# Performance work log

Measured on AMD Instinct MI355X. Metric: run time of the kernel, lower is better.

Reference implementation:

```python
import jax, jax.numpy as jnp
import numpy as np

EPS = 1e-5  # torch LayerNorm default

def _ln(x):
    # LayerNorm over last dim, no affine (elementwise_affine=False)
    m = jnp.mean(x, axis=-1, keepdims=True)
    v = jnp.var(x, axis=-1, keepdims=True)
    return (x - m) / jnp.sqrt(v + EPS)

def _build_orthogonal(phi):
    """Orthogonal matrix of the 'X' RBS circuit on d qubits (unary subspace).
    phi has 2d-3 angles: a descending diagonal of d-1 adjacent Givens rotations
    followed by an ascending diagonal of d-2. Each RBS(theta) acts on coords
    (k, k+1) as [[cos, sin], [-sin, cos]]."""
    d = (phi.shape[0] + 3) // 2
    W = jnp.eye(d, dtype=phi.dtype)
    wires = list(range(d - 1)) + list(range(d - 3, -1, -1))  # 2d-3 gates
    for g, k in enumerate(wires):
        c, s = jnp.cos(phi[g]), jnp.sin(phi[g])
        rk, rk1 = W[k], W[k + 1]
        W = W.at[k].set(c * rk + s * rk1)
        W = W.at[k + 1].set(-s * rk + c * rk1)
    return W

def setup_inputs() -> dict:
    key = jax.random.key(0)
    ks = jax.random.split(key, 8)
    B, N, E, H, dh = 16, 1024, 512, 8, 64
    return {
        "x": jax.random.normal(ks[0], (B, N, E), jnp.float32),
        "Wv": jax.random.normal(ks[1], (H, dh, dh), jnp.float32) / np.sqrt(dh).astype(np.float32),
        "bv": jnp.zeros((H, dh), jnp.float32),
        "phi": jax.random.uniform(ks[2], (H, 2 * dh - 3), jnp.float32, 0.0, 2.0 * np.pi),
        "W1": jax.random.normal(ks[3], (E, E), jnp.float32) / np.sqrt(E).astype(np.float32),
        "b1": jnp.zeros((E,), jnp.float32),
        "W2": jax.random.normal(ks[4], (E, E), jnp.float32) / np.sqrt(E).astype(np.float32),
        "b2": jnp.zeros((E,), jnp.float32),
    }

def reference(x, Wv, bv, phi, W1, b1, W2, b2):
    B, N, E = x.shape
    H = Wv.shape[0]
    dh = E // H
    xn = _ln(x)                                    # norm1
    xh = xn.reshape(B, N, H, dh)                   # per-head slices
    Worth = jax.vmap(_build_orthogonal)(phi)       # [H, dh, dh]
    # per-head value projection (nn.Linear weights stored as [in, out])
    V = jnp.einsum('bnhd,hde->bnhe', xh, Wv) + bv  # [B,N,H,dh]
    # quantum attention scores: loader(x_j) -> W(phi) -> inverse loader(x_i),
    # rescaled by |x_i||x_j|  ==  A_ij = x_i^T W(phi) x_j
    A = jnp.einsum('bnhd,hde,bmhe->bhnm', xh, Worth, xh)
    P = jax.nn.softmax(A / np.float32(np.sqrt(dh)), axis=-1)
    attn = jnp.einsum('bhnm,bmhe->bnhe', P, V)
    head_out = _ln(attn + xh)                      # per-head LN over dh
    res = head_out.reshape(B, N, E) + x            # MHA + residual
    # merger: Linear -> GELU(exact) -> Linear on norm2(res)
    h = jax.nn.gelu(_ln(res) @ W1 + b1, approximate=False) @ W2 + b2
    return h + res
```

## Files before the change

kernel.cpp:

```cpp
#include <hip/hip_runtime.h>
#include <hip/hip_bf16.h>
#include <math.h>

#define B_  16
#define N_  1024
#define E_  512
#define H_  8

typedef __attribute__((ext_vector_type(8)))  __bf16 bf16x8;
typedef __attribute__((ext_vector_type(4)))  float  f32x4;
typedef __attribute__((ext_vector_type(16))) float  f32x16;
typedef __attribute__((ext_vector_type(4)))  unsigned int u32x4;

struct alignas(16) bf8pack { __hip_bfloat16 v[8]; };
struct alignas(8)  bf4pack { __hip_bfloat16 v[4]; };

static __device__ __forceinline__ float bf2f(__hip_bfloat16 x) { return __bfloat162float(x); }
static __device__ __forceinline__ __hip_bfloat16 f2bf(float x) { return __float2bfloat16(x); }

static __device__ __forceinline__ unsigned pkbf(float lo, float hi) {
    unsigned r;
    asm("v_cvt_pk_bf16_f32 %0, %1, %2" : "=v"(r) : "v"(lo), "v"(hi));
    return r;
}
static __device__ __forceinline__ void swap32(unsigned &a, unsigned &b) {
    asm("v_permlane32_swap_b32 %0, %1" : "+v"(a), "+v"(b));
}
static __device__ __forceinline__ void gload16(const __hip_bfloat16* g, __hip_bfloat16* l) {
    __builtin_amdgcn_global_load_lds(
        (const __attribute__((address_space(1))) unsigned*)g,
        (__attribute__((address_space(3))) unsigned*)l, 16, 0, 0);
}
#define MFMA32(a, b, c) __builtin_amdgcn_mfma_f32_32x32x16_bf16((a), (b), (c), 0, 0, 0)
#define MFMA16(a, b, c) __builtin_amdgcn_mfma_f32_16x16x32_bf16((a), (b), (c), 0, 0, 0)

__global__ __launch_bounds__(64) void k_worth(const float* __restrict__ phi,
                                              const float* __restrict__ Wv,
                                              __hip_bfloat16* __restrict__ worth_t,
                                              __hip_bfloat16* __restrict__ wvt) {
    const float SCL = 0.18033688011112042f;
    __shared__ float W[64 * 65];
    int h = blockIdx.x;
    int t = threadIdx.x;
    for (int i = 0; i < 64; ++i) W[i * 65 + t] = (i == t) ? 1.0f : 0.0f;
    for (int g = 0; g < 125; ++g) {
        int k = (g < 63) ? g : (124 - g);
        float ph = phi[h * 125 + g];
        float c = cosf(ph), s = sinf(ph);
        float a  = W[k * 65 + t];
        float b  = W[(k + 1) * 65 + t];
        W[k * 65 + t]       =  c * a + s * b;
        W[(k + 1) * 65 + t] = -s * a + c * b;
    }
    for (int d = 0; d < 64; ++d)
        worth_t[h * 4096 + t * 64 + d] = f2bf(W[d * 65 + t] * SCL);
    for (int d = 0; d < 64; ++d)
        wvt[h * 4096 + t * 64 + d] = f2bf(Wv[h * 4096 + d * 64 + t]);
}

__global__ __launch_bounds__(256) void k_transpose(const float* __restrict__ W1,
                                                   const float* __restrict__ W2,
                                                   __hip_bfloat16* __restrict__ w1t,
                                                   __hip_bfloat16* __restrict__ w2t) {
    const float* src = blockIdx.y ? W2 : W1;
    __hip_bfloat16* dst = blockIdx.y ? w2t : w1t;
    int i0 = (blockIdx.x & 7) * 64, o0 = (blockIdx.x >> 3) * 64;
    int tid = threadIdx.x;
    __shared__ float ts[64][65];
    int r = tid >> 4, c4 = (tid & 15) * 4;
#pragma unroll
    for (int j4 = 0; j4 < 4; ++j4) {
        float4 v = *reinterpret_cast<const float4*>(&src[(size_t)(i0 + r + 16 * j4) * 512 + o0 + c4]);
        ts[r + 16 * j4][c4 + 0] = v.x; ts[r + 16 * j4][c4 + 1] = v.y;
        ts[r + 16 * j4][c4 + 2] = v.z; ts[r + 16 * j4][c4 + 3] = v.w;
    }
    __syncthreads();
    int o = tid >> 3, cg = tid & 7;
#pragma unroll
    for (int half = 0; half < 2; ++half) {
        int oo = o + 32 * half;
        bf8pack p;
#pragma unroll
        for (int j = 0; j < 8; ++j) p.v[j] = f2bf(ts[cg * 8 + j][oo]);
        *reinterpret_cast<bf8pack*>(&dst[(size_t)(o0 + oo) * 512 + i0 + cg * 8]) = p;
    }
}

template <typename T>
__global__ __launch_bounds__(256) void k_ln(const T* __restrict__ in,
                                            __hip_bfloat16* __restrict__ out) {
    int w = threadIdx.x >> 6, l = threadIdx.x & 63;
    size_t row = (size_t)blockIdx.x * 4 + w;
    float vv[8];
    if constexpr (sizeof(T) == 4) {
        const float* p = (const float*)in + row * 512 + l * 8;
        float4 v0 = *reinterpret_cast<const float4*>(p);
        float4 v1 = *reinterpret_cast<const float4*>(p + 4);
        vv[0]=v0.x; vv[1]=v0.y; vv[2]=v0.z; vv[3]=v0.w;
        vv[4]=v1.x; vv[5]=v1.y; vv[6]=v1.z; vv[7]=v1.w;
    } else {
        const __hip_bfloat16* p = (const __hip_bfloat16*)in + row * 512 + l * 8;
        bf16x8 u = *reinterpret_cast<const bf16x8*>(p);
#pragma unroll
        for (int j = 0; j < 8; ++j) vv[j] = (float)u[j];
    }
    float s = 0.f, sq = 0.f;
#pragma unroll
    for (int j = 0; j < 8; ++j) { s += vv[j]; sq += vv[j] * vv[j]; }
#pragma unroll
    for (int o = 32; o >= 1; o >>= 1) { s += __shfl_xor(s, o); sq += __shfl_xor(sq, o); }
    float mean = s * (1.0f / 512.0f);
    float var  = sq * (1.0f / 512.0f) - mean * mean;
    float rstd = rsqrtf(var + 1e-5f);
    bf8pack ob;
#pragma unroll
    for (int j = 0; j < 8; ++j) ob.v[j] = f2bf((vv[j] - mean) * rstd);
    *reinterpret_cast<bf8pack*>(out + row * 512 + l * 8) = ob;
}

__global__ __launch_bounds__(256) void k_proj(const __hip_bfloat16* __restrict__ xn,
                                              const __hip_bfloat16* __restrict__ worth_t,
                                              const __hip_bfloat16* __restrict__ wvt,
                                              const float* __restrict__ bv,
                                              __hip_bfloat16* __restrict__ xw,
                                              __hip_bfloat16* __restrict__ vt) {
    int h = blockIdx.y, rt = blockIdx.x;
    int tid = threadIdx.x, w = tid >> 6, l = tid & 63;
    int lr = l & 15, lg = l >> 4;
    int nw = rt * 64 + w * 16;
    int b  = (rt * 64) >> 10;
    int n0 = (rt * 64) & 1023;
    size_t bh = (size_t)b * H_ + h;

    const __hip_bfloat16* xp = xn + (size_t)(nw + lr) * 512 + h * 64 + lg * 8;
    bf16x8 xf0 = *reinterpret_cast<const bf16x8*>(xp);
    bf16x8 xf1 = *reinterpret_cast<const bf16x8*>(xp + 32);

    f32x4 accw[4] = {}, accv[4] = {};
#pragma unroll
    for (int g = 0; g < 4; ++g) {
        const __hip_bfloat16* wp = worth_t + h * 4096 + (g * 16 + lr) * 64 + lg * 8;
        accw[g] = MFMA16(*reinterpret_cast<const bf16x8*>(wp), xf0, accw[g]);
        accw[g] = MFMA16(*reinterpret_cast<const bf16x8*>(wp + 32), xf1, accw[g]);
        const __hip_bfloat16* vp = wvt + h * 4096 + (g * 16 + lr) * 64 + lg * 8;
        accv[g] = MFMA16(xf0, *reinterpret_cast<const bf16x8*>(vp), accv[g]);
        accv[g] = MFMA16(xf1, *reinterpret_cast<const bf16x8*>(vp + 32), accv[g]);
    }
#pragma unroll
    for (int g = 0; g < 4; ++g) {
        bf4pack pw;
#pragma unroll
        for (int r = 0; r < 4; ++r) pw.v[r] = f2bf(accw[g][r]);
        *reinterpret_cast<bf4pack*>(xw + (bh * N_ + n0 + w * 16 + lr) * 64 + g * 16 + lg * 4) = pw;
        float bb = bv[h * 64 + g * 16 + lr];
        bf4pack pv;
#pragma unroll
        for (int r = 0; r < 4; ++r) pv.v[r] = f2bf(accv[g][r] + bb);
        *reinterpret_cast<bf4pack*>(vt + (bh * 64 + g * 16 + lr) * N_ + n0 + w * 16 + lg * 4) = pv;
    }
}

__global__ __launch_bounds__(512, 4) void k_attn(const __hip_bfloat16* __restrict__ xn,
                                                 const __hip_bfloat16* __restrict__ xw,
                                                 const __hip_bfloat16* __restrict__ vt,
                                                 const float* __restrict__ x,
                                                 __hip_bfloat16* __restrict__ res) {
    int h = blockIdx.x, b = blockIdx.z;
    int tid = threadIdx.x;
    int w = tid >> 6, l = tid & 63;
    int lq = l & 31, hi = l >> 5;
    int so = lq & 7;
    int q0 = blockIdx.y * 256 + w * 32;
    size_t bh = (size_t)b * H_ + h;

    __shared__ __hip_bfloat16 kb[3][4096];
    __shared__ __hip_bfloat16 vb[3][4096];
    __shared__ float lred[8][32];

    int rloc = w * 8 + (l >> 3);
    int gs = ((l & 7) ^ (rloc & 7)) << 3;
    const __hip_bfloat16* ksrc = xn + ((size_t)b * N_ + rloc) * 512 + h * 64 + gs;
    const __hip_bfloat16* vsrc = vt + (bh * 64 + rloc) * N_ + gs;

#define STAGE(q, m0) do { \
        gload16(ksrc + (size_t)(m0) * 512, &kb[q][w * 512]); \
        gload16(vsrc + (m0), &vb[q][w * 512]); } while (0)
#define TILE_BAR(nvm) do { \
        asm volatile("s_waitcnt vmcnt(" #nvm ")" ::: "memory"); \
        __builtin_amdgcn_s_barrier(); \
        __builtin_amdgcn_sched_barrier(0); } while (0)

    const __hip_bfloat16* qp = xw + (bh * N_ + q0 + lq) * 64 + 8 * hi;
    bf16x8 qf0 = *reinterpret_cast<const bf16x8*>(qp);
    bf16x8 qf1 = *reinterpret_cast<const bf16x8*>(qp + 16);
    bf16x8 qf2 = *reinterpret_cast<const bf16x8*>(qp + 32);
    bf16x8 qf3 = *reinterpret_cast<const bf16x8*>(qp + 48);

    f32x16 o0 = {}, o1 = {};
    float l_run = 0.f;

    auto tile_body = [&](int qc) {
        const __hip_bfloat16* kc = &kb[qc][0];
        const __hip_bfloat16* vc = &vb[qc][0];
        f32x16 s0 = {}, s1 = {};
        __builtin_amdgcn_s_setprio(1);
#pragma unroll
        for (int kd = 0; kd < 4; ++kd) {
            bf16x8 qf = (kd == 0) ? qf0 : (kd == 1) ? qf1 : (kd == 2) ? qf2 : qf3;
            int sl = ((kd * 2 + hi) ^ so) << 3;
            bf16x8 ka0 = *reinterpret_cast<const bf16x8*>(kc + lq * 64 + sl);
            bf16x8 ka1 = *reinterpret_cast<const bf16x8*>(kc + (lq + 32) * 64 + sl);
            s0 = MFMA32(ka0, qf, s0);
            s1 = MFMA32(ka1, qf, s1);
        }
        __builtin_amdgcn_s_setprio(0);
#pragma unroll
        for (int i = 0; i < 16; ++i) {
            s0[i] = __builtin_amdgcn_exp2f(s0[i]);
            s1[i] = __builtin_amdgcn_exp2f(s1[i]);
        }
        float ls = 0.f;
#pragma unroll
        for (int i = 0; i < 16; ++i) ls += s0[i] + s1[i];
        l_run += ls;
        bf16x8 pa[4];
        {
            unsigned u0 = pkbf(s0[0], s0[1]), u1 = pkbf(s0[2], s0[3]);
            unsigned u2 = pkbf(s0[4], s0[5]), u3 = pkbf(s0[6], s0[7]);
            swap32(u0, u2); swap32(u1, u3);
            u32x4 uu = {u0, u1, u2, u3};
            pa[0] = __builtin_bit_cast(bf16x8, uu);
        }
        {
            unsigned u0 = pkbf(s0[8], s0[9]),   u1 = pkbf(s0[10], s0[11]);
            unsigned u2 = pkbf(s0[12], s0[13]), u3 = pkbf(s0[14], s0[15]);
            swap32(u0, u2); swap32(u1, u3);
            u32x4 uu = {u0, u1, u2, u3};
            pa[1] = __builtin_bit_cast(bf16x8, uu);
        }
        {
            unsigned u0 = pkbf(s1[0], s1[1]), u1 = pkbf(s1[2], s1[3]);
            unsigned u2 = pkbf(s1[4], s1[5]), u3 = pkbf(s1[6], s1[7]);
            swap32(u0, u2); swap32(u1, u3);
            u32x4 uu = {u0, u1, u2, u3};
            pa[2] = __builtin_bit_cast(bf16x8, uu);
        }
        {
            unsigned u0 = pkbf(s1[8], s1[9]),   u1 = pkbf(s1[10], s1[11]);
            unsigned u2 = pkbf(s1[12], s1[13]), u3 = pkbf(s1[14], s1[15]);
            swap32(u0, u2); swap32(u1, u3);
            u32x4 uu = {u0, u1, u2, u3};
            pa[3] = __builtin_bit_cast(bf16x8, uu);
        }
        __builtin_amdgcn_s_setprio(1);
#pragma unroll
        for (int ks = 0; ks < 4; ++ks) {
            int sl = ((ks * 2 + hi) ^ so) << 3;
            bf16x8 v0 = *reinterpret_cast<const bf16x8*>(vc + lq * 64 + sl);
            bf16x8 v1 = *reinterpret_cast<const bf16x8*>(vc + (lq + 32) * 64 + sl);
            o0 = MFMA32(pa[ks], v0, o0);
            o1 = MFMA32(pa[ks], v1, o1);
        }
        __builtin_amdgcn_s_setprio(0);
    };

    STAGE(0, 0);
    STAGE(1, 64);
    TILE_BAR(0);

    int qc = 0;
    for (int t = 0; t < 14; ++t) {
        int qn = qc + 2; if (qn >= 3) qn -= 3;
        STAGE(qn, (t + 2) * 64);
        tile_body(qc);
        TILE_BAR(2);
        qc = (qc == 2) ? 0 : qc + 1;
    }
    tile_body(qc);
    TILE_BAR(0);
    tile_body(0);

    float lt = l_run + __shfl_xor(l_run, 32);
    if (hi == 0) lred[w][lq] = 1.0f / lt;
#pragma unroll
    for (int r = 0; r < 16; ++r) {
        int qr = (r & 3) + 8 * (r >> 2) + 4 * hi;
        float li = lred[w][qr];
        size_t base = ((size_t)b * N_ + q0 + qr) * 512 + h * 64;
        float t0 = o0[r] * li + bf2f(xn[base + lq]);
        float t1 = o1[r] * li + bf2f(xn[base + 32 + lq]);
        float s1v = t0 + t1, s2v = t0 * t0 + t1 * t1;
#pragma unroll
        for (int off = 16; off >= 1; off >>= 1) { s1v += __shfl_xor(s1v, off); s2v += __shfl_xor(s2v, off); }
        float mean = s1v * (1.0f / 64.0f);
        float var  = s2v * (1.0f / 64.0f) - mean * mean;
        float rstd = rsqrtf(var + 1e-5f);
        res[base + lq]      = f2bf((t0 - mean) * rstd + x[base + lq]);
        res[base + 32 + lq] = f2bf((t1 - mean) * rstd + x[base + 32 + lq]);
    }
#undef STAGE
#undef TILE_BAR
}

template <int MODE>
__global__ __launch_bounds__(256) void k_gemm(const __hip_bfloat16* __restrict__ A,
                                              const __hip_bfloat16* __restrict__ Bt,
                                              const float* __restrict__ bias,
                                              const __hip_bfloat16* __restrict__ resid,
                                              __hip_bfloat16* __restrict__ outb,
                                              float* __restrict__ outf) {
    int m0 = blockIdx.x * 128, nn0 = blockIdx.y * 64;
    int tid = threadIdx.x, w = tid >> 6, l = tid & 63;
    int lr = l & 15, lg = l >> 4;
    __shared__ __hip_bfloat16 bs[64 * 512];

#pragma unroll
    for (int i = 0; i < 16; ++i) {
        int row = w * 16 + i;
        gload16(Bt + (size_t)(nn0 + row) * 512 + ((l ^ (row & 7)) << 3),
                &bs[row * 512]);
    }
    __syncthreads();

    f32x4 acc0[4] = {}, acc1[4] = {};
    const __hip_bfloat16* ap0 = A + (size_t)(m0 + w * 32 + lr) * 512 + lg * 8;
    const __hip_bfloat16* ap1 = ap0 + 16 * 512;
#pragma unroll
    for (int k = 0; k < 512; k += 32) {
        bf16x8 a0 = *reinterpret_cast<const bf16x8*>(ap0 + k);
        bf16x8 a1 = *reinterpret_cast<const bf16x8*>(ap1 + k);
#pragma unroll
        for (int g = 0; g < 4; ++g) {
            int row = g * 16 + lr;
            bf16x8 bf = *reinterpret_cast<const bf16x8*>(
                bs + row * 512 + ((((k >> 3) + lg) ^ (row & 7)) << 3));
            acc0[g] = MFMA16(a0, bf, acc0[g]);
            acc1[g] = MFMA16(a1, bf, acc1[g]);
        }
    }
#pragma unroll
    for (int g = 0; g < 4; ++g) {
        int col = nn0 + g * 16 + lr;
        float bb = bias[col];
#pragma unroll
        for (int r = 0; r < 4; ++r) {
            int row0 = m0 + w * 32 + lg * 4 + r;
            float v0 = acc0[g][r] + bb;
            float v1 = acc1[g][r] + bb;
            if (MODE == 0) {
                float g0 = 0.5f * v0 * (1.0f + erff(v0 * 0.70710678118654752f));
                float g1 = 0.5f * v1 * (1.0f + erff(v1 * 0.70710678118654752f));
                outb[(size_t)row0 * 512 + col] = f2bf(g0);
                outb[(size_t)(row0 + 16) * 512 + col] = f2bf(g1);
            } else {
                size_t i0 = (size_t)row0 * 512 + col;
                size_t i1 = (size_t)(row0 + 16) * 512 + col;
                outf[i0] = v0 + bf2f(resid[i0]);
                outf[i1] = v1 + bf2f(resid[i1]);
            }
        }
    }
}

extern "C" void kernel_launch(void* const* d_in, const int* in_sizes, int n_in,
                              void* d_out, int out_size, void* d_ws, size_t ws_size,
                              hipStream_t stream) {
    const float* x   = (const float*)d_in[0];
    const float* Wv  = (const float*)d_in[1];
    const float* bv  = (const float*)d_in[2];
    const float* phi = (const float*)d_in[3];
    const float* W1  = (const float*)d_in[4];
    const float* b1  = (const float*)d_in[5];
    const float* W2  = (const float*)d_in[6];
    const float* b2  = (const float*)d_in[7];
    float* out = (float*)d_out;

    char* ws = (char*)d_ws;
    __hip_bfloat16* worth_t = (__hip_bfloat16*)(ws + 0);
    __hip_bfloat16* wvt     = (__hip_bfloat16*)(ws + 65536);
    __hip_bfloat16* w1t     = (__hip_bfloat16*)(ws + 131072);
    __hip_bfloat16* w2t     = (__hip_bfloat16*)(ws + 655360);
    __hip_bfloat16* xn      = (__hip_bfloat16*)(ws + 1179648);
    __hip_bfloat16* xw      = (__hip_bfloat16*)(ws + 17956864);
    __hip_bfloat16* vt      = (__hip_bfloat16*)(ws + 34734080);
    __hip_bfloat16* res     = (__hip_bfloat16*)(ws + 51511296);
    __hip_bfloat16* xn2     = (__hip_bfloat16*)(ws + 68288512);
    __hip_bfloat16* y1      = (__hip_bfloat16*)(ws + 85065728);

    k_worth<<<dim3(8), dim3(64), 0, stream>>>(phi, Wv, worth_t, wvt);
    k_transpose<<<dim3(64, 2), dim3(256), 0, stream>>>(W1, W2, w1t, w2t);
    k_ln<float><<<dim3(4096), dim3(256), 0, stream>>>(x, xn);
    k_proj<<<dim3(256, 8), dim3(256), 0, stream>>>(xn, worth_t, wvt, bv, xw, vt);
    k_attn<<<dim3(8, 4, 16), dim3(512), 0, stream>>>(xn, xw, vt, x, res);
    k_ln<__hip_bfloat16><<<dim3(4096), dim3(256), 0, stream>>>(res, xn2);
    k_gemm<0><<<dim3(128, 8), dim3(256), 0, stream>>>(xn2, w1t, b1, nullptr, y1, nullptr);
    k_gemm<1><<<dim3(128, 8), dim3(256), 0, stream>>>(y1, w2t, b2, res, nullptr, out);
}
```

Before: 178.5 us.

## Restage attention and GEMM pipelines with double-buffered LDS and fast GELU

The attention kernel moves from a 3-deep ring of 64-key tiles to double-buffered 128-key tiles, which halves the barrier count and changes the V swizzle to 16 slots. The GEMM kernel no longer loads the whole 64x512 B panel into LDS up front. It streams it in 128-wide K chunks with double buffering, which lowers LDS use so more blocks fit per CU (launch bounds set to 5). The exact erff GELU is replaced with an Abramowitz-Stegun polynomial approximation using exp2, which cheapens the epilogue but adds about 1e-7 absolute error.

```diff
diff --git a/kernel.cpp b/kernel.cpp
--- a/kernel.cpp
+++ b/kernel.cpp
@@ -33,6 +33,17 @@
 }
 #define MFMA32(a, b, c) __builtin_amdgcn_mfma_f32_32x32x16_bf16((a), (b), (c), 0, 0, 0)
 #define MFMA16(a, b, c) __builtin_amdgcn_mfma_f32_16x16x32_bf16((a), (b), (c), 0, 0, 0)
+
+static __device__ __forceinline__ float gelu_f(float v) {
+    float z = fabsf(v) * 0.70710678118654752f;
+    float t = 1.0f / fmaf(0.3275911f, z, 1.0f);
+    float p = t * fmaf(t, fmaf(t, fmaf(t, fmaf(t, 1.061405429f, -1.453152027f),
+                                       1.421413741f), -0.284496736f), 0.254829592f);
+    float e = __builtin_amdgcn_exp2f(-z * z * 1.4426950408889634f);
+    float erf = 1.0f - p * e;
+    erf = copysignf(erf, v);
+    return 0.5f * v * (1.0f + erf);
+}
 
 __global__ __launch_bounds__(64) void k_worth(const float* __restrict__ phi,
                                               const float* __restrict__ Wv,
@@ -169,24 +180,28 @@
     int tid = threadIdx.x;
     int w = tid >> 6, l = tid & 63;
     int lq = l & 31, hi = l >> 5;
-    int so = lq & 7;
     int q0 = blockIdx.y * 256 + w * 32;
     size_t bh = (size_t)b * H_ + h;
 
-    __shared__ __hip_bfloat16 kb[3][4096];
-    __shared__ __hip_bfloat16 vb[3][4096];
+    __shared__ __hip_bfloat16 kb[2][128 * 64];
+    __shared__ __hip_bfloat16 vb[2][64 * 128];
     __shared__ float lred[8][32];
 
-    int rloc = w * 8 + (l >> 3);
-    int gs = ((l & 7) ^ (rloc & 7)) << 3;
-    const __hip_bfloat16* ksrc = xn + ((size_t)b * N_ + rloc) * 512 + h * 64 + gs;
-    const __hip_bfloat16* vsrc = vt + (bh * 64 + rloc) * N_ + gs;
-
-#define STAGE(q, m0) do { \
-        gload16(ksrc + (size_t)(m0) * 512, &kb[q][w * 512]); \
-        gload16(vsrc + (m0), &vb[q][w * 512]); } while (0)
-#define TILE_BAR(nvm) do { \
-        asm volatile("s_waitcnt vmcnt(" #nvm ")" ::: "memory"); \
+    int krow = w * 16 + (l >> 3);
+    const __hip_bfloat16* ksrc = xn + ((size_t)b * N_ + krow) * 512 + h * 64
+                               + (((l & 7) ^ (krow & 7)) << 3);
+    int vrow0 = w * 8 + (l >> 4);
+    int vrow1 = vrow0 + 4;
+    const __hip_bfloat16* vsrc0 = vt + (bh * 64 + vrow0) * N_ + (((l & 15) ^ (vrow0 & 15)) << 3);
+    const __hip_bfloat16* vsrc1 = vt + (bh * 64 + vrow1) * N_ + (((l & 15) ^ (vrow1 & 15)) << 3);
+
+#define STAGE(t) do { int bf_ = (t) & 1; \
+        gload16(ksrc + (size_t)((t) * 128) * 512,     &kb[bf_][(w * 16) * 64]); \
+        gload16(ksrc + (size_t)((t) * 128 + 8) * 512, &kb[bf_][(w * 16 + 8) * 64]); \
+        gload16(vsrc0 + (t) * 128, &vb[bf_][(w * 8) * 128]); \
+        gload16(vsrc1 + (t) * 128, &vb[bf_][(w * 8 + 4) * 128]); } while (0)
+#define TILE_BAR() do { \
+        asm volatile("s_waitcnt vmcnt(0)" ::: "memory"); \
         __builtin_amdgcn_s_barrier(); \
         __builtin_amdgcn_sched_barrier(0); } while (0)
 
@@ -198,16 +213,18 @@
 
     f32x16 o0 = {}, o1 = {};
     float l_run = 0.f;
-
-    auto tile_body = [&](int qc) {
-        const __hip_bfloat16* kc = &kb[qc][0];
-        const __hip_bfloat16* vc = &vb[qc][0];
+    int kso = lq & 7;
+    int vso = lq & 15;
+
+    auto body = [&](int bf_, int mm) {
+        const __hip_bfloat16* kc = &kb[bf_][mm * 64 * 64];
+        const __hip_bfloat16* vc = &vb[bf_][0];
         f32x16 s0 = {}, s1 = {};
         __builtin_amdgcn_s_setprio(1);
 #pragma unroll
         for (int kd = 0; kd < 4; ++kd) {
             bf16x8 qf = (kd == 0) ? qf0 : (kd == 1) ? qf1 : (kd == 2) ? qf2 : qf3;
-            int sl = ((kd * 2 + hi) ^ so) << 3;
+            int sl = ((kd * 2 + hi) ^ kso) << 3;
             bf16x8 ka0 = *reinterpret_cast<const bf16x8*>(kc + lq * 64 + sl);
             bf16x8 ka1 = *reinterpret_cast<const bf16x8*>(kc + (lq + 32) * 64 + sl);
             s0 = MFMA32(ka0, qf, s0);
@@ -255,30 +272,25 @@
         __builtin_amdgcn_s_setprio(1);
 #pragma unroll
         for (int ks = 0; ks < 4; ++ks) {
-            int sl = ((ks * 2 + hi) ^ so) << 3;
-            bf16x8 v0 = *reinterpret_cast<const bf16x8*>(vc + lq * 64 + sl);
-            bf16x8 v1 = *reinterpret_cast<const bf16x8*>(vc + (lq + 32) * 64 + sl);
+            int sl = ((mm * 8 + ks * 2 + hi) ^ vso) << 3;
+            bf16x8 v0 = *reinterpret_cast<const bf16x8*>(vc + lq * 128 + sl);
+            bf16x8 v1 = *reinterpret_cast<const bf16x8*>(vc + (lq + 32) * 128 + sl);
             o0 = MFMA32(pa[ks], v0, o0);
             o1 = MFMA32(pa[ks], v1, o1);
         }
         __builtin_amdgcn_s_setprio(0);
     };
 
-    STAGE(0, 0);
-    STAGE(1, 64);
-    TILE_BAR(0);
-
-    int qc = 0;
-    for (int t = 0; t < 14; ++t) {
-        int qn = qc + 2; if (qn >= 3) qn -= 3;
-        STAGE(qn, (t + 2) * 64);
-        tile_body(qc);
-        TILE_BAR(2);
-        qc = (qc == 2) ? 0 : qc + 1;
-    }
-    tile_body(qc);
-    TILE_BAR(0);
-    tile_body(0);
+    STAGE(0);
+    TILE_BAR();
+    for (int t = 0; t < 7; ++t) {
+        STAGE(t + 1);
+        body(t & 1, 0);
+        body(t & 1, 1);
+        TILE_BAR();
+    }
+    body(1, 0);
+    body(1, 1);
 
     float lt = l_run + __shfl_xor(l_run, 32);
     if (hi == 0) lred[w][lq] = 1.0f / lt;
@@ -303,41 +315,60 @@
 }
 
 template <int MODE>
-__global__ __launch_bounds__(256) void k_gemm(const __hip_bfloat16* __restrict__ A,
-                                              const __hip_bfloat16* __restrict__ Bt,
-                                              const float* __restrict__ bias,
-                                              const __hip_bfloat16* __restrict__ resid,
-                                              __hip_bfloat16* __restrict__ outb,
-                                              float* __restrict__ outf) {
+__global__ __launch_bounds__(256, 5) void k_gemm(const __hip_bfloat16* __restrict__ A,
+                                                 const __hip_bfloat16* __restrict__ Bt,
+                                                 const float* __restrict__ bias,
+                                                 const __hip_bfloat16* __restrict__ resid,
+                                                 __hip_bfloat16* __restrict__ outb,
+                                                 float* __restrict__ outf) {
     int m0 = blockIdx.x * 128, nn0 = blockIdx.y * 64;
     int tid = threadIdx.x, w = tid >> 6, l = tid & 63;
     int lr = l & 15, lg = l >> 4;
-    __shared__ __hip_bfloat16 bs[64 * 512];
-
-#pragma unroll
-    for (int i = 0; i < 16; ++i) {
-        int row = w * 16 + i;
-        gload16(Bt + (size_t)(nn0 + row) * 512 + ((l ^ (row & 7)) << 3),
-                &bs[row * 512]);
-    }
-    __syncthreads();
+    __shared__ __hip_bfloat16 bs[2][64 * 128];
+
+    int srow = w * 16 + (l >> 4);
+    int sslot = l & 15;
+
+#define GSTAGE(c) do { \
+        _Pragma("unroll") \
+        for (int i_ = 0; i_ < 4; ++i_) { \
+            int row_ = srow + i_ * 4; \
+            gload16(Bt + (size_t)(nn0 + row_) * 512 + (c) * 128 + ((sslot ^ (row_ & 15)) << 3), \
+                    &bs[(c) & 1][(w * 16 + i_ * 4) * 128]); \
+        } } while (0)
+
+    GSTAGE(0);
+    asm volatile("s_waitcnt vmcnt(0)" ::: "memory");
+    __builtin_amdgcn_s_barrier();
+    __builtin_amdgcn_sched_barrier(0);
 
     f32x4 acc0[4] = {}, acc1[4] = {};
     const __hip_bfloat16* ap0 = A + (size_t)(m0 + w * 32 + lr) * 512 + lg * 8;
     const __hip_bfloat16* ap1 = ap0 + 16 * 512;
 #pragma unroll
-    for (int k = 0; k < 512; k += 32) {
-        bf16x8 a0 = *reinterpret_cast<const bf16x8*>(ap0 + k);
-        bf16x8 a1 = *reinterpret_cast<const bf16x8*>(ap1 + k);
-#pragma unroll
-        for (int g = 0; g < 4; ++g) {
-            int row = g * 16 + lr;
-            bf16x8 bf = *reinterpret_cast<const bf16x8*>(
-                bs + row * 512 + ((((k >> 3) + lg) ^ (row & 7)) << 3));
-            acc0[g] = MFMA16(a0, bf, acc0[g]);
-            acc1[g] = MFMA16(a1, bf, acc1[g]);
-        }
-    }
+    for (int c = 0; c < 4; ++c) {
+        if (c < 3) GSTAGE(c + 1);
+        const __hip_bfloat16* bc = &bs[c & 1][0];
+#pragma unroll
+        for (int kk = 0; kk < 4; ++kk) {
+            bf16x8 a0 = *reinterpret_cast<const bf16x8*>(ap0 + c * 128 + kk * 32);
+            bf16x8 a1 = *reinterpret_cast<const bf16x8*>(ap1 + c * 128 + kk * 32);
+#pragma unroll
+            for (int g = 0; g < 4; ++g) {
+                int row = g * 16 + lr;
+                bf16x8 bf = *reinterpret_cast<const bf16x8*>(
+                    bc + row * 128 + (((kk * 4 + lg) ^ (row & 15)) << 3));
+                acc0[g] = MFMA16(a0, bf, acc0[g]);
+                acc1[g] = MFMA16(a1, bf, acc1[g]);
+            }
+        }
+        if (c < 3) {
+            asm volatile("s_waitcnt vmcnt(0)" ::: "memory");
+            __builtin_amdgcn_s_barrier();
+            __builtin_amdgcn_sched_barrier(0);
+        }
+    }
+#undef GSTAGE
 #pragma unroll
     for (int g = 0; g < 4; ++g) {
         int col = nn0 + g * 16 + lr;
@@ -348,10 +379,8 @@
             float v0 = acc0[g][r] + bb;
             float v1 = acc1[g][r] + bb;
             if (MODE == 0) {
-                float g0 = 0.5f * v0 * (1.0f + erff(v0 * 0.70710678118654752f));
-                float g1 = 0.5f * v1 * (1.0f + erff(v1 * 0.70710678118654752f));
-                outb[(size_t)row0 * 512 + col] = f2bf(g0);
-                outb[(size_t)(row0 + 16) * 512 + col] = f2bf(g1);
+                outb[(size_t)row0 * 512 + col] = f2bf(gelu_f(v0));
+                outb[(size_t)(row0 + 16) * 512 + col] = f2bf(gelu_f(v1));
             } else {
                 size_t i0 = (size_t)row0 * 512 + col;
                 size_t i1 = (size_t)(row0 + 16) * 512 + col;
```

Result: no change. 179.4 us (+0.5%).
